# Kernel tuning notes

Hardware: AMD Instinct MI355X
Metric: run time of the kernel (lower is better)

The kernel has to match this reference:

```python
import jax, jax.numpy as jnp
import numpy as np


def setup_inputs() -> dict:
    key = jax.random.key(0)
    k1, k2, k3, k4 = jax.random.split(key, 4)
    bs, ts0, tsk, f, nf = 1024, 32, 32, 64, 64
    return {
        "x_0": jax.random.normal(k1, (bs, ts0, f), dtype=jnp.float32),
        "x_k": jax.random.normal(k2, (bs, tsk, f), dtype=jnp.float32),
        # Conv1d weight as used: (num_filters, in_ch=1, ts_0, ts_k)
        "weight": jax.random.normal(k3, (nf, 1, ts0, tsk), dtype=jnp.float32) * 0.05,
        "bias": jax.random.normal(k4, (nf,), dtype=jnp.float32) * 0.05,
    }


def reference(x_0, x_k, weight, bias):
    bs, ts0, f = x_0.shape
    _, tsk, _ = x_k.shape
    # Outer-product interaction: (bs, f, ts_0, ts_k). This is the large HBM
    # intermediate (268 MB at these shapes) that a fused kernel would avoid.
    z = jnp.einsum('btf,byf->bfty', x_0, x_k)
    # Faithful row-major view to (bs, 1, ts_0, f*ts_k) as in torch .view.
    z = z.reshape(bs, 1, ts0, f * tsk)
    # Conv with kernel (ts_0, ts_k), stride ts_k along width; kernel height
    # equals input height so output is (bs, nf, 1, f). (Height stride is
    # irrelevant since exactly one vertical position exists.)
    out = jax.lax.conv_general_dilated(
        z, weight,
        window_strides=(tsk, tsk),
        padding='VALID',
        dimension_numbers=('NCHW', 'OIHW', 'NCHW'),
    )
    out = out + bias[None, :, None, None]
    return jnp.squeeze(out)  # (bs, num_filters, f)
```

## Files before the change

### kernel.cpp

```cpp
#include <hip/hip_runtime.h>


constexpr int ST0 = 36;

__global__ __launch_bounds__(1024)
__attribute__((amdgpu_waves_per_eu(4, 4)))
void cin_fused(const float* __restrict__ x0,
               const float* __restrict__ xk,
               const float* __restrict__ W,
               const float* __restrict__ bias,
               float* __restrict__ out)
{
    __shared__ __align__(16) float xkL[4][32 * 64];
    __shared__ __align__(16) float x0T[4][64 * ST0];
    __shared__ __align__(16) float Gt[4][64 * 64];

    const int tid = threadIdx.x;
    const int b0  = blockIdx.x * 4;
    const int n   = tid & 63;
    const int wv  = tid >> 6;
    const int r0  = 2 * wv;

    const float4* xksrc = reinterpret_cast<const float4*>(xk + (size_t)b0 * 2048);
    const float4* x0src = reinterpret_cast<const float4*>(x0 + (size_t)b0 * 2048);
    const float4 k0 = xksrc[tid];
    const float4 k1 = xksrc[tid + 1024];
    const float4 a0 = x0src[tid];
    const float4 a1 = x0src[tid + 1024];

    float w0reg[32], w1reg[32];
    {
        const float4* wp = reinterpret_cast<const float4*>(W + ((size_t)n * 32 + r0) * 32);
        #pragma unroll
        for (int q = 0; q < 8; ++q) {
            const float4 v = wp[q];
            w0reg[4*q+0] = v.x; w0reg[4*q+1] = v.y; w0reg[4*q+2] = v.z; w0reg[4*q+3] = v.w;
        }
        #pragma unroll
        for (int q = 0; q < 8; ++q) {
            const float4 v = wp[8 + q];
            w1reg[4*q+0] = v.x; w1reg[4*q+1] = v.y; w1reg[4*q+2] = v.z; w1reg[4*q+3] = v.w;
        }
    }

    {
        const int kb = tid >> 9;
        const int u  = tid & 511;
        reinterpret_cast<float4*>(xkL[kb    ])[u] = k0;
        reinterpret_cast<float4*>(xkL[kb + 2])[u] = k1;
        const int st  = u >> 4;
        const int sf4 = u & 15;
        const int sts = st ^ (4 * (sf4 & 7));
        float* r0w = &x0T[kb    ][(4 * sf4) * ST0];
        float* r1w = &x0T[kb + 2][(4 * sf4) * ST0];
        r0w[0 * ST0 + sts] = a0.x; r0w[1 * ST0 + sts] = a0.y;
        r0w[2 * ST0 + sts] = a0.z; r0w[3 * ST0 + sts] = a0.w;
        r1w[0 * ST0 + sts] = a1.x; r1w[1 * ST0 + sts] = a1.y;
        r1w[2 * ST0 + sts] = a1.z; r1w[3 * ST0 + sts] = a1.w;
    }
    __syncthreads();

    for (int kb = 0; kb < 4; ++kb) {
        const float* p = &xkL[kb][4 * wv];
        float a00 = 0.f, a01 = 0.f, a10 = 0.f, a11 = 0.f;
        #pragma unroll
        for (int q = 0; q < 4; ++q) {
            float4 kv[8];
            #pragma unroll
            for (int m = 0; m < 8; ++m)
                kv[m] = *reinterpret_cast<const float4*>(p + (q * 8 + m) * 64);
            #pragma unroll
            for (int m = 0; m < 8; ++m) {
                const int j = q * 8 + m;
                a00 = fmaf(w0reg[j], kv[m].x, a00);
                a01 = fmaf(w0reg[j], kv[m].y, a01);
                a10 = fmaf(w1reg[j], kv[m].z, a10);
                a11 = fmaf(w1reg[j], kv[m].w, a11);
            }
        }
        Gt[kb][(r0     ) * 64 + n] = a00;
        Gt[kb][(32 + r0) * 64 + n] = a01;
        Gt[kb][(r0 + 1 ) * 64 + n] = a10;
        Gt[kb][(33 + r0) * 64 + n] = a11;
    }
    __syncthreads();

    {
        const int kb = tid >> 8;
        const int t2 = tid & 255;
        const int n0 = (t2 >> 4) * 4;
        const int w0 = (t2 & 15) * 4;
        const int h  = w0 >> 5;
        const int t0 = w0 & 31;

        const float4 bv = *reinterpret_cast<const float4*>(bias + n0);
        float acc[4][4];
        #pragma unroll
        for (int i = 0; i < 4; ++i) { acc[0][i] = bv.x; acc[1][i] = bv.y; acc[2][i] = bv.z; acc[3][i] = bv.w; }

        #pragma unroll
        for (int r = 0; r < 32; ++r) {
            const int swz = 4 * ((r >> 1) & 7);
            const float4 xv = *reinterpret_cast<const float4*>(
                &x0T[kb][(2 * r + h) * ST0 + (t0 ^ swz)]);
            const float4 gv = *reinterpret_cast<const float4*>(
                &Gt[kb][(h * 32 + r) * 64 + n0]);
            acc[0][0] = fmaf(gv.x, xv.x, acc[0][0]);
            acc[0][1] = fmaf(gv.x, xv.y, acc[0][1]);
            acc[0][2] = fmaf(gv.x, xv.z, acc[0][2]);
            acc[0][3] = fmaf(gv.x, xv.w, acc[0][3]);
            acc[1][0] = fmaf(gv.y, xv.x, acc[1][0]);
            acc[1][1] = fmaf(gv.y, xv.y, acc[1][1]);
            acc[1][2] = fmaf(gv.y, xv.z, acc[1][2]);
            acc[1][3] = fmaf(gv.y, xv.w, acc[1][3]);
            acc[2][0] = fmaf(gv.z, xv.x, acc[2][0]);
            acc[2][1] = fmaf(gv.z, xv.y, acc[2][1]);
            acc[2][2] = fmaf(gv.z, xv.z, acc[2][2]);
            acc[2][3] = fmaf(gv.z, xv.w, acc[2][3]);
            acc[3][0] = fmaf(gv.w, xv.x, acc[3][0]);
            acc[3][1] = fmaf(gv.w, xv.y, acc[3][1]);
            acc[3][2] = fmaf(gv.w, xv.z, acc[3][2]);
            acc[3][3] = fmaf(gv.w, xv.w, acc[3][3]);
        }

        float* ob = out + (size_t)(b0 + kb) * 4096;
        #pragma unroll
        for (int e = 0; e < 4; ++e) {
            *reinterpret_cast<float4*>(&ob[(n0 + e) * 64 + w0]) =
                make_float4(acc[e][0], acc[e][1], acc[e][2], acc[e][3]);
        }
    }
}

extern "C" void kernel_launch(void* const* d_in, const int* in_sizes, int n_in,
                              void* d_out, int out_size, void* d_ws, size_t ws_size,
                              hipStream_t stream) {
    const float* x0   = (const float*)d_in[0];
    const float* xk   = (const float*)d_in[1];
    const float* W    = (const float*)d_in[2];
    const float* bias = (const float*)d_in[3];
    float* out = (float*)d_out;

    cin_fused<<<dim3(256), dim3(1024), 0, stream>>>(x0, xk, W, bias, out);
}
```

Baseline: 90.54 us.

## Read xk directly from global and use 8x8 register tiles on four waves

Drops the xk shared-memory staging: each wave now reads its xk float4 slice straight from global memory, using a wave-uniform index from readfirstlane. The G intermediate moves to a padded row layout (stride 136) with a different swizzle. The second contraction now runs on only four waves (wv%5==0), each lane computing an 8x8 output tile, which raises register reuse but leaves 12 of 16 waves idle during that phase. The trade is less LDS traffic and fewer LDS reads per FMA against much less parallelism in the final stage and repeated global reads of xk.

```diff
diff --git a/kernel.cpp b/kernel.cpp
--- a/kernel.cpp
+++ b/kernel.cpp
@@ -2,6 +2,8 @@
 
 
 constexpr int ST0 = 36;
+constexpr int GR  = 136;
+constexpr int GB  = 32 * GR;
 
 __global__ __launch_bounds__(1024)
 __attribute__((amdgpu_waves_per_eu(4, 4)))
@@ -11,26 +13,22 @@
                const float* __restrict__ bias,
                float* __restrict__ out)
 {
-    __shared__ __align__(16) float xkL[4][32 * 64];
-    __shared__ __align__(16) float x0T[4][64 * ST0];
-    __shared__ __align__(16) float Gt[4][64 * 64];
+    __shared__ __align__(16) float x0T[4 * 64 * ST0];
+    __shared__ __align__(16) float Gs[4 * GB];
 
-    const int tid = threadIdx.x;
-    const int b0  = blockIdx.x * 4;
-    const int n   = tid & 63;
-    const int wv  = tid >> 6;
-    const int r0  = 2 * wv;
+    const int tid  = threadIdx.x;
+    const int b0   = blockIdx.x * 4;
+    const int lane = tid & 63;
+    const int wv   = tid >> 6;
+    const int r0   = 2 * wv;
 
-    const float4* xksrc = reinterpret_cast<const float4*>(xk + (size_t)b0 * 2048);
     const float4* x0src = reinterpret_cast<const float4*>(x0 + (size_t)b0 * 2048);
-    const float4 k0 = xksrc[tid];
-    const float4 k1 = xksrc[tid + 1024];
     const float4 a0 = x0src[tid];
     const float4 a1 = x0src[tid + 1024];
 
     float w0reg[32], w1reg[32];
     {
-        const float4* wp = reinterpret_cast<const float4*>(W + ((size_t)n * 32 + r0) * 32);
+        const float4* wp = reinterpret_cast<const float4*>(W + ((size_t)lane * 32 + r0) * 32);
         #pragma unroll
         for (int q = 0; q < 8; ++q) {
             const float4 v = wp[q];
@@ -44,31 +42,30 @@
     }
 
     {
-        const int kb = tid >> 9;
-        const int u  = tid & 511;
-        reinterpret_cast<float4*>(xkL[kb    ])[u] = k0;
-        reinterpret_cast<float4*>(xkL[kb + 2])[u] = k1;
+        const int kb  = tid >> 9;
+        const int u   = tid & 511;
         const int st  = u >> 4;
         const int sf4 = u & 15;
         const int sts = st ^ (4 * (sf4 & 7));
-        float* r0w = &x0T[kb    ][(4 * sf4) * ST0];
-        float* r1w = &x0T[kb + 2][(4 * sf4) * ST0];
-        r0w[0 * ST0 + sts] = a0.x; r0w[1 * ST0 + sts] = a0.y;
-        r0w[2 * ST0 + sts] = a0.z; r0w[3 * ST0 + sts] = a0.w;
-        r1w[0 * ST0 + sts] = a1.x; r1w[1 * ST0 + sts] = a1.y;
-        r1w[2 * ST0 + sts] = a1.z; r1w[3 * ST0 + sts] = a1.w;
+        float* rA = &x0T[(kb    ) * 64 * ST0 + (4 * sf4) * ST0];
+        float* rB = &x0T[(kb + 2) * 64 * ST0 + (4 * sf4) * ST0];
+        rA[0 * ST0 + sts] = a0.x; rA[1 * ST0 + sts] = a0.y;
+        rA[2 * ST0 + sts] = a0.z; rA[3 * ST0 + sts] = a0.w;
+        rB[0 * ST0 + sts] = a1.x; rB[1 * ST0 + sts] = a1.y;
+        rB[2 * ST0 + sts] = a1.z; rB[3 * ST0 + sts] = a1.w;
     }
     __syncthreads();
 
+    const int su = __builtin_amdgcn_readfirstlane(wv);
     for (int kb = 0; kb < 4; ++kb) {
-        const float* p = &xkL[kb][4 * wv];
+        const float4* pk4 = reinterpret_cast<const float4*>(xk + (size_t)(b0 + kb) * 2048);
         float a00 = 0.f, a01 = 0.f, a10 = 0.f, a11 = 0.f;
         #pragma unroll
         for (int q = 0; q < 4; ++q) {
             float4 kv[8];
             #pragma unroll
             for (int m = 0; m < 8; ++m)
-                kv[m] = *reinterpret_cast<const float4*>(p + (q * 8 + m) * 64);
+                kv[m] = pk4[(q * 8 + m) * 16 + su];
             #pragma unroll
             for (int m = 0; m < 8; ++m) {
                 const int j = q * 8 + m;
@@ -78,56 +75,59 @@
                 a11 = fmaf(w1reg[j], kv[m].w, a11);
             }
         }
-        Gt[kb][(r0     ) * 64 + n] = a00;
-        Gt[kb][(32 + r0) * 64 + n] = a01;
-        Gt[kb][(r0 + 1 ) * 64 + n] = a10;
-        Gt[kb][(33 + r0) * 64 + n] = a11;
+        float* gb = &Gs[kb * GB];
+        gb[(r0    ) * GR +      lane] = a00;
+        gb[(r0    ) * GR + 68 + lane] = a01;
+        gb[(r0 + 1) * GR +      lane] = a10;
+        gb[(r0 + 1) * GR + 68 + lane] = a11;
     }
     __syncthreads();
 
-    {
-        const int kb = tid >> 8;
-        const int t2 = tid & 255;
-        const int n0 = (t2 >> 4) * 4;
-        const int w0 = (t2 & 15) * 4;
-        const int h  = w0 >> 5;
-        const int t0 = w0 & 31;
+    if (wv % 5 == 0) {
+        const int ckb = wv / 5;
+        const int l   = lane;
+        const int n0  = (l >> 3) * 8;
+        const int w0c = (l & 7) * 8;
+        const int h   = w0c >> 5;
+        const int t0  = w0c & 31;
 
-        const float4 bv = *reinterpret_cast<const float4*>(bias + n0);
-        float acc[4][4];
+        const float4 bva = *reinterpret_cast<const float4*>(bias + n0);
+        const float4 bvb = *reinterpret_cast<const float4*>(bias + n0 + 4);
+
+        float acc[8][8];
         #pragma unroll
-        for (int i = 0; i < 4; ++i) { acc[0][i] = bv.x; acc[1][i] = bv.y; acc[2][i] = bv.z; acc[3][i] = bv.w; }
-
-        #pragma unroll
-        for (int r = 0; r < 32; ++r) {
-            const int swz = 4 * ((r >> 1) & 7);
-            const float4 xv = *reinterpret_cast<const float4*>(
-                &x0T[kb][(2 * r + h) * ST0 + (t0 ^ swz)]);
-            const float4 gv = *reinterpret_cast<const float4*>(
-                &Gt[kb][(h * 32 + r) * 64 + n0]);
-            acc[0][0] = fmaf(gv.x, xv.x, acc[0][0]);
-            acc[0][1] = fmaf(gv.x, xv.y, acc[0][1]);
-            acc[0][2] = fmaf(gv.x, xv.z, acc[0][2]);
-            acc[0][3] = fmaf(gv.x, xv.w, acc[0][3]);
-            acc[1][0] = fmaf(gv.y, xv.x, acc[1][0]);
-            acc[1][1] = fmaf(gv.y, xv.y, acc[1][1]);
-            acc[1][2] = fmaf(gv.y, xv.z, acc[1][2]);
-            acc[1][3] = fmaf(gv.y, xv.w, acc[1][3]);
-            acc[2][0] = fmaf(gv.z, xv.x, acc[2][0]);
-            acc[2][1] = fmaf(gv.z, xv.y, acc[2][1]);
-            acc[2][2] = fmaf(gv.z, xv.z, acc[2][2]);
-            acc[2][3] = fmaf(gv.z, xv.w, acc[2][3]);
-            acc[3][0] = fmaf(gv.w, xv.x, acc[3][0]);
-            acc[3][1] = fmaf(gv.w, xv.y, acc[3][1]);
-            acc[3][2] = fmaf(gv.w, xv.z, acc[3][2]);
-            acc[3][3] = fmaf(gv.w, xv.w, acc[3][3]);
+        for (int i = 0; i < 8; ++i) {
+            acc[0][i] = bva.x; acc[1][i] = bva.y; acc[2][i] = bva.z; acc[3][i] = bva.w;
+            acc[4][i] = bvb.x; acc[5][i] = bvb.y; acc[6][i] = bvb.z; acc[7][i] = bvb.w;
         }
 
-        float* ob = out + (size_t)(b0 + kb) * 4096;
+        const float* xbase = &x0T[ckb * 64 * ST0];
+        const float* gbase = &Gs[ckb * GB + h * 68];
+
+        #pragma unroll 4
+        for (int r = 0; r < 32; ++r) {
+            const int fi = 2 * r + h;
+            const int p  = 4 * ((fi >> 2) & 7);
+            const float4 xa = *reinterpret_cast<const float4*>(&xbase[fi * ST0 + (t0 ^ p)]);
+            const float4 xb = *reinterpret_cast<const float4*>(&xbase[fi * ST0 + ((t0 + 4) ^ p)]);
+            const float4 g0 = *reinterpret_cast<const float4*>(&gbase[r * GR + n0]);
+            const float4 g1 = *reinterpret_cast<const float4*>(&gbase[r * GR + n0 + 4]);
+            const float ge[8] = {g0.x, g0.y, g0.z, g0.w, g1.x, g1.y, g1.z, g1.w};
+            const float xv[8] = {xa.x, xa.y, xa.z, xa.w, xb.x, xb.y, xb.z, xb.w};
+            #pragma unroll
+            for (int e = 0; e < 8; ++e)
+                #pragma unroll
+                for (int i = 0; i < 8; ++i)
+                    acc[e][i] = fmaf(ge[e], xv[i], acc[e][i]);
+        }
+
+        float* ob = out + (size_t)(b0 + ckb) * 4096;
         #pragma unroll
-        for (int e = 0; e < 4; ++e) {
-            *reinterpret_cast<float4*>(&ob[(n0 + e) * 64 + w0]) =
+        for (int e = 0; e < 8; ++e) {
+            *reinterpret_cast<float4*>(&ob[(n0 + e) * 64 + w0c]) =
                 make_float4(acc[e][0], acc[e][1], acc[e][2], acc[e][3]);
+            *reinterpret_cast<float4*>(&ob[(n0 + e) * 64 + w0c + 4]) =
+                make_float4(acc[e][4], acc[e][5], acc[e][6], acc[e][7]);
         }
     }
 }
```

Result: slower. 95.67 us (+5.7%).
